# Optimization experiments

Measured on AMD Instinct MI355X. Metric: run time of the kernel, lower is better.

Reference implementation:

```python
import jax, jax.numpy as jnp
import numpy as np

N = 100000      # nodes
E = 1600000     # edges (avg degree 16)
F_IN = 128      # in_feats
H = 128         # n_hidden
C = 40          # n_classes


def setup_inputs() -> dict:
    key = jax.random.key(0)
    ks = jax.random.split(key, 11)
    s = 0.05
    return {
        "x": jax.random.normal(ks[0], (N, F_IN), jnp.float32),
        "edge_index": jax.random.randint(ks[1], (2, E), 0, N, jnp.int32),
        # layer 1: SAGEConv(F_IN, H); lin_l has bias, lin_r has none (PyG default)
        "Wl1": jax.random.normal(ks[2], (F_IN, H), jnp.float32) * s,
        "bl1": jnp.zeros((H,), jnp.float32),
        "Wr1": jax.random.normal(ks[3], (F_IN, H), jnp.float32) * s,
        # layer 2: SAGEConv(H, H)
        "Wl2": jax.random.normal(ks[4], (H, H), jnp.float32) * s,
        "bl2": jnp.zeros((H,), jnp.float32),
        "Wr2": jax.random.normal(ks[5], (H, H), jnp.float32) * s,
        # layer 3: SAGEConv(H, C)
        "Wl3": jax.random.normal(ks[6], (H, C), jnp.float32) * s,
        "bl3": jnp.zeros((C,), jnp.float32),
        "Wr3": jax.random.normal(ks[7], (H, C), jnp.float32) * s,
    }


def _sage_conv(x, src, dst, Wl, bl, Wr):
    # PyG SAGEConv (aggr='mean', root_weight=True):
    #   out[i] = lin_l( mean_{j->i} x[j] ) + lin_r( x[i] )
    msgs = x[src]                                            # [E, d] irregular gather
    agg = jax.ops.segment_sum(msgs, dst, num_segments=N)     # [N, d]
    deg = jax.ops.segment_sum(jnp.ones((src.shape[0], 1), x.dtype), dst,
                              num_segments=N)                # [N, 1]
    agg = agg / jnp.maximum(deg, 1.0)                        # mean aggregation
    return agg @ Wl + bl + x @ Wr


def reference(x, edge_index, Wl1, bl1, Wr1, Wl2, bl2, Wr2, Wl3, bl3, Wr3):
    src, dst = edge_index[0], edge_index[1]
    h = jax.nn.relu(_sage_conv(x, src, dst, Wl1, bl1, Wr1))   # dropout is identity in eval
    h = jax.nn.relu(_sage_conv(h, src, dst, Wl2, bl2, Wr2))
    return _sage_conv(h, src, dst, Wl3, bl3, Wr3)             # [N, C]
```

## Files before the change

### kernel.cpp

```cpp
#include <hip/hip_runtime.h>

using u16 = unsigned short;
using u32 = unsigned int;
using u8 = unsigned char;
typedef __attribute__((ext_vector_type(8))) short short8;
typedef __attribute__((ext_vector_type(4))) float f32x4;

static inline int idiv_up(long a, long b) { return (int)((a + b - 1) / b); }

#define NBUCK 256
#define ECHUNK 8192
#define CAPE 9216

__device__ __forceinline__ float bflo(u32 p) { return __uint_as_float(p << 16); }
__device__ __forceinline__ float bfhi(u32 p) { return __uint_as_float(p & 0xffff0000u); }
__device__ __forceinline__ u32 f2bf1(float f) {
    u32 x = __float_as_uint(f);
    return (x + 0x7fffu + ((x >> 16) & 1u)) >> 16;
}
__device__ __forceinline__ u32 pack2(float lo, float hi) {
    return f2bf1(lo) | (f2bf1(hi) << 16);
}

__global__ __launch_bounds__(256) void k_cast(const float* __restrict__ x,
                                              u32* __restrict__ xb, long nelem) {
    long i = ((long)blockIdx.x * 256 + threadIdx.x) * 8;
    if (i >= nelem) return;
    float4 v0 = *(const float4*)(x + i);
    float4 v1 = *(const float4*)(x + i + 4);
    uint4 o;
    o.x = pack2(v0.x, v0.y);
    o.y = pack2(v0.z, v0.w);
    o.z = pack2(v1.x, v1.y);
    o.w = pack2(v1.z, v1.w);
    *(uint4*)(xb + (i >> 1)) = o;
}

__global__ __launch_bounds__(256) void k_wprepall(const float* __restrict__ Wl1,
                                                  const float* __restrict__ Wr1,
                                                  const float* __restrict__ Wl2,
                                                  const float* __restrict__ Wr2,
                                                  const float* __restrict__ Wl3,
                                                  const float* __restrict__ Wr3,
                                                  u16* __restrict__ wp1,
                                                  u16* __restrict__ wp2,
                                                  u16* __restrict__ wp3) {
    const int b = blockIdx.x;
    if (b < 32) {
        const float* Wl = (b < 16) ? Wl1 : Wl2;
        const float* Wr = (b < 16) ? Wr1 : Wr2;
        u16* wp = (b < 16) ? wp1 : wp2;
        const int gid = (b & 15) * 256 + threadIdx.x;
        const int tile = gid >> 6, l = gid & 63;
        const int t = tile >> 3, s = tile & 7;
        const int n = t * 16 + (l & 15);
        const int k0 = s * 32 + (l >> 4) * 8;
        u32 w[4];
#pragma unroll
        for (int p = 0; p < 4; ++p) {
            const int ka = k0 + 2 * p, kb = ka + 1;
            const float va = (ka < 128) ? Wl[ka * 128 + n] : Wr[(ka - 128) * 128 + n];
            const float vb = (kb < 128) ? Wl[kb * 128 + n] : Wr[(kb - 128) * 128 + n];
            w[p] = pack2(va, vb);
        }
        uint4 o = {w[0], w[1], w[2], w[3]};
        *(uint4*)(wp + (size_t)gid * 8) = o;
    } else {
        const int gid = (b - 32) * 256 + threadIdx.x;
        if (gid >= 20 * 64) return;
        const int tile = gid >> 6, l = gid & 63;
        const int t = tile >> 2, s = tile & 3;
        const int c = t * 16 + (l & 15);
        const int k0 = s * 32 + (l >> 4) * 8;
        u32 w[4];
#pragma unroll
        for (int p = 0; p < 4; ++p) {
            const int ka = k0 + 2 * p, kb = ka + 1;
            const float va = (c < 40) ? Wl3[ka * 40 + c] : Wr3[ka * 40 + (c - 40)];
            const float vb = (c < 40) ? Wl3[kb * 40 + c] : Wr3[kb * 40 + (c - 40)];
            w[p] = pack2(va, vb);
        }
        uint4 o = {w[0], w[1], w[2], w[3]};
        *(uint4*)(wp3 + (size_t)gid * 8) = o;
    }
}

__global__ __launch_bounds__(256) void k_bucket(const int* __restrict__ src,
                                                const int* __restrict__ dst,
                                                int* __restrict__ cursor,
                                                u32* __restrict__ stage,
                                                int E, int rangeSize) {
    __shared__ u32 s_pay[ECHUNK];
    __shared__ u8 s_bk[ECHUNK];
    __shared__ int s_cnt[NBUCK];
    __shared__ int s_base[NBUCK];
    __shared__ int s_off[NBUCK];
    s_cnt[threadIdx.x] = 0;
    __syncthreads();
    const long e0 = (long)blockIdx.x * ECHUNK;
    const int cnt = (int)(((long)E - e0 < ECHUNK) ? (long)E - e0 : ECHUNK);
    for (int j = threadIdx.x; j < cnt; j += 256) {
        const int d = __builtin_nontemporal_load(&dst[e0 + j]);
        const int s = __builtin_nontemporal_load(&src[e0 + j]);
        const int b = d / rangeSize;
        s_pay[j] = (u32)s | ((u32)(d - b * rangeSize) << 17);
        s_bk[j] = (u8)b;
        atomicAdd(&s_cnt[b], 1);
    }
    __syncthreads();
    {
        const int c = s_cnt[threadIdx.x];
        s_base[threadIdx.x] = c ? atomicAdd(&cursor[threadIdx.x], c) : 0;
        s_off[threadIdx.x] = 0;
    }
    __syncthreads();
    for (int j = threadIdx.x; j < cnt; j += 256) {
        const int b = s_bk[j];
        const int p = atomicAdd(&s_off[b], 1);
        stage[(size_t)b * CAPE + s_base[b] + p] = s_pay[j];
    }
}

__global__ __launch_bounds__(256) void k_csrlds(const u32* __restrict__ stage,
                                                const int* __restrict__ cursor,
                                                int* __restrict__ rowptr,
                                                float* __restrict__ invd,
                                                int* __restrict__ col,
                                                int rangeSize, int n) {
    __shared__ int s_cnt[512];
    __shared__ int s_cur[512];
    __shared__ int s_col[CAPE];
    __shared__ int wt[4];
    __shared__ int sh_gbase;
    const int b = blockIdx.x;
    const int t = threadIdx.x;
    const int g0 = b * rangeSize;
    const size_t rd = (size_t)b * CAPE;

    {
        const int v = cursor[t];
        const int lane = t & 63, wid = t >> 6;
        int incl = v;
        for (int off = 1; off < 64; off <<= 1) {
            int u = __shfl_up(incl, off, 64);
            if (lane >= off) incl += u;
        }
        if (lane == 63) wt[wid] = incl;
        __syncthreads();
        int woff = 0;
        for (int w = 0; w < wid; ++w) woff += wt[w];
        if (t == b) sh_gbase = woff + incl - v;
    }
    __syncthreads();
    const int cntb = cursor[b];
    const int gbase = sh_gbase;

    for (int i = t; i < rangeSize; i += 256) s_cnt[i] = 0;
    __syncthreads();

    for (int i = t; i < cntb; i += 256)
        atomicAdd(&s_cnt[stage[rd + i] >> 17], 1);
    __syncthreads();

    const int i0 = 2 * t, i1 = 2 * t + 1;
    const int c0 = (i0 < rangeSize) ? s_cnt[i0] : 0;
    const int c1 = (i1 < rangeSize) ? s_cnt[i1] : 0;
    const int sum = c0 + c1;
    const int lane = t & 63, wid = t >> 6;
    int incl = sum;
    for (int off = 1; off < 64; off <<= 1) {
        int u = __shfl_up(incl, off, 64);
        if (lane >= off) incl += u;
    }
    __syncthreads();
    if (lane == 63) wt[wid] = incl;
    __syncthreads();
    int woff = 0;
    for (int w = 0; w < wid; ++w) woff += wt[w];
    const int excl = woff + incl - sum;
    if (i0 < rangeSize) {
        s_cur[i0] = excl;
        const int g = g0 + i0;
        if (g <= n) rowptr[g] = gbase + excl;
        if (g < n) invd[g] = 1.0f / fmaxf((float)c0, 1.0f);
    }
    if (i1 < rangeSize) {
        s_cur[i1] = excl + c0;
        const int g = g0 + i1;
        if (g <= n) rowptr[g] = gbase + excl + c0;
        if (g < n) invd[g] = 1.0f / fmaxf((float)c1, 1.0f);
    }
    __syncthreads();

    for (int i = t; i < cntb; i += 256) {
        const u32 v = stage[rd + i];
        const int p = atomicAdd(&s_cur[v >> 17], 1);
        s_col[p] = (int)(v & 0x1FFFFu);
    }
    __syncthreads();

    for (int i = t; i < cntb; i += 256) col[gbase + i] = s_col[i];
}

#define ACC4(A, V)                                                     \
    A.x += bflo(V.x); A.y += bfhi(V.x); A.z += bflo(V.y); A.w += bfhi(V.y);

__global__ __launch_bounds__(256, 6) void k_aggmm(const u16* __restrict__ xb,
                                                  const int* __restrict__ rowptr,
                                                  const int* __restrict__ col,
                                                  const float* __restrict__ invd,
                                                  const u16* __restrict__ wp,
                                                  const float* __restrict__ bl,
                                                  u16* __restrict__ outb, int n) {
    __shared__ __align__(16) u16 s_a[64][136];
    const int row0 = blockIdx.x * 64;
    const int tid = threadIdx.x;

    const int l32 = tid & 31;
#pragma unroll
    for (int it = 0; it < 8; ++it) {
        const int r = it * 8 + (tid >> 5);
        const int node = row0 + r;
        float4 a0 = {0.f, 0.f, 0.f, 0.f};
        float4 a1 = {0.f, 0.f, 0.f, 0.f};
        float inv = 0.f;
        if (node < n) {
            inv = invd[node];
            const int s0 = rowptr[node], s1 = rowptr[node + 1];
            for (int cb = s0; cb < s1; cb += 32) {
                const int cnt = min(32, s1 - cb);
                const int cc = (cb + l32 < s1) ? col[cb + l32] : 0;
                int j = 0;
                for (; j + 8 <= cnt; j += 8) {
                    const int n0 = __shfl(cc, j, 32);
                    const int n1 = __shfl(cc, j + 1, 32);
                    const int n2 = __shfl(cc, j + 2, 32);
                    const int n3 = __shfl(cc, j + 3, 32);
                    const int n4 = __shfl(cc, j + 4, 32);
                    const int n5 = __shfl(cc, j + 5, 32);
                    const int n6 = __shfl(cc, j + 6, 32);
                    const int n7 = __shfl(cc, j + 7, 32);
                    const uint2 v0 = *(const uint2*)(xb + (size_t)n0 * 128 + 4 * l32);
                    const uint2 v1 = *(const uint2*)(xb + (size_t)n1 * 128 + 4 * l32);
                    const uint2 v2 = *(const uint2*)(xb + (size_t)n2 * 128 + 4 * l32);
                    const uint2 v3 = *(const uint2*)(xb + (size_t)n3 * 128 + 4 * l32);
                    const uint2 v4 = *(const uint2*)(xb + (size_t)n4 * 128 + 4 * l32);
                    const uint2 v5 = *(const uint2*)(xb + (size_t)n5 * 128 + 4 * l32);
                    const uint2 v6 = *(const uint2*)(xb + (size_t)n6 * 128 + 4 * l32);
                    const uint2 v7 = *(const uint2*)(xb + (size_t)n7 * 128 + 4 * l32);
                    ACC4(a0, v0); ACC4(a1, v1); ACC4(a0, v2); ACC4(a1, v3);
                    ACC4(a0, v4); ACC4(a1, v5); ACC4(a0, v6); ACC4(a1, v7);
                }
                for (; j + 4 <= cnt; j += 4) {
                    const int n0 = __shfl(cc, j, 32);
                    const int n1 = __shfl(cc, j + 1, 32);
                    const int n2 = __shfl(cc, j + 2, 32);
                    const int n3 = __shfl(cc, j + 3, 32);
                    const uint2 v0 = *(const uint2*)(xb + (size_t)n0 * 128 + 4 * l32);
                    const uint2 v1 = *(const uint2*)(xb + (size_t)n1 * 128 + 4 * l32);
                    const uint2 v2 = *(const uint2*)(xb + (size_t)n2 * 128 + 4 * l32);
                    const uint2 v3 = *(const uint2*)(xb + (size_t)n3 * 128 + 4 * l32);
                    ACC4(a0, v0); ACC4(a1, v1); ACC4(a0, v2); ACC4(a1, v3);
                }
                for (; j < cnt; ++j) {
                    const int nn = __shfl(cc, j, 32);
                    const uint2 v = *(const uint2*)(xb + (size_t)nn * 128 + 4 * l32);
                    ACC4(a0, v);
                }
            }
        }
        uint2 o;
        o.x = pack2((a0.x + a1.x) * inv, (a0.y + a1.y) * inv);
        o.y = pack2((a0.z + a1.z) * inv, (a0.w + a1.w) * inv);
        *(uint2*)(&s_a[r][4 * l32]) = o;
    }
    __syncthreads();

    const int l64 = tid & 63;
    const int w = tid >> 6;
    const int rloc = w * 16 + (l64 & 15);
    const int q = l64 >> 4;
    const int rowc = min(row0 + rloc, n - 1);

    f32x4 acc[8];
#pragma unroll
    for (int t = 0; t < 8; ++t) acc[t] = (f32x4){0.f, 0.f, 0.f, 0.f};

#pragma unroll
    for (int s = 0; s < 8; ++s) {
        const short8 a = (s < 4)
            ? *(const short8*)(&s_a[rloc][s * 32 + q * 8])
            : *(const short8*)(xb + (size_t)rowc * 128 + (s - 4) * 32 + q * 8);
#pragma unroll
        for (int t = 0; t < 8; ++t) {
            const short8 b = *(const short8*)(wp + ((size_t)(t * 8 + s) * 64 + l64) * 8);
            acc[t] = __builtin_amdgcn_mfma_f32_16x16x32_bf16(a, b, acc[t], 0, 0, 0);
        }
    }

    const int cb16 = l64 & 15;
    const int rowl = w * 16 + q * 4;
#pragma unroll
    for (int t = 0; t < 8; ++t) {
        const float bias = bl[t * 16 + cb16];
#pragma unroll
        for (int r = 0; r < 4; ++r) {
            const float o = fmaxf(acc[t][r] + bias, 0.f);
            s_a[rowl + r][t * 16 + cb16] = (u16)f2bf1(o);
        }
    }
    __syncthreads();
#pragma unroll
    for (int it = 0; it < 4; ++it) {
        const int idx = tid + it * 256;
        const int r = idx >> 4, c8 = idx & 15;
        const int row = row0 + r;
        if (row < n)
            *(uint4*)(outb + (size_t)row * 128 + c8 * 8) = *(const uint4*)(&s_a[r][c8 * 8]);
    }
}

__global__ __launch_bounds__(256, 4) void k_mm40f(const u16* __restrict__ hb,
                                                  const u16* __restrict__ wp,
                                                  const float* __restrict__ bl,
                                                  u16* __restrict__ t40b,
                                                  float* __restrict__ r40, int n) {
    __shared__ __align__(16) u16 s_a[64][136];
    const int row0 = blockIdx.x * 64;
    const int tid = threadIdx.x;

#pragma unroll
    for (int it = 0; it < 4; ++it) {
        const int idx = tid + it * 256;
        const int r = idx >> 4, c8 = idx & 15;
        const int row = row0 + r;
        uint4 v = {0u, 0u, 0u, 0u};
        if (row < n) v = *(const uint4*)(hb + (size_t)row * 128 + c8 * 8);
        *(uint4*)(&s_a[r][c8 * 8]) = v;
    }
    __syncthreads();

    const int l = tid & 63;
    const int w = tid >> 6;
    const int rloc = w * 16 + (l & 15);
    const int q = l >> 4;

    short8 afr[4];
#pragma unroll
    for (int s = 0; s < 4; ++s)
        afr[s] = *(const short8*)(&s_a[rloc][s * 32 + q * 8]);

    f32x4 acc[5];
#pragma unroll
    for (int t = 0; t < 5; ++t) acc[t] = (f32x4){0.f, 0.f, 0.f, 0.f};

#pragma unroll
    for (int t = 0; t < 5; ++t) {
#pragma unroll
        for (int s = 0; s < 4; ++s) {
            const short8 b = *(const short8*)(wp + ((size_t)(t * 4 + s) * 64 + l) * 8);
            acc[t] = __builtin_amdgcn_mfma_f32_16x16x32_bf16(afr[s], b, acc[t], 0, 0, 0);
        }
    }

    const int rowb = row0 + w * 16 + q * 4;
#pragma unroll
    for (int t = 0; t < 5; ++t) {
        const int c = t * 16 + (l & 15);
        const float bias = (c >= 40) ? bl[c - 40] : 0.f;
#pragma unroll
        for (int r = 0; r < 4; ++r) {
            const int row = rowb + r;
            if (row < n) {
                if (c < 40)
                    t40b[(size_t)row * 40 + c] = (u16)f2bf1(acc[t][r]);
                else
                    r40[(size_t)row * 40 + (c - 40)] = acc[t][r] + bias;
            }
        }
    }
}

__global__ __launch_bounds__(256) void k_agg40(const u16* __restrict__ t40b,
                                               const float* __restrict__ r40,
                                               const int* __restrict__ rowptr,
                                               const int* __restrict__ col,
                                               const float* __restrict__ invd,
                                               float* __restrict__ out, int n) {
    const int tt = blockIdx.x * 256 + threadIdx.x;
    const int node = tt >> 4;
    if (node >= n) return;
    const int l = tt & 15;
    const bool act = l < 10;
    const int s0 = rowptr[node], s1 = rowptr[node + 1];
    float4 a0 = {0.f, 0.f, 0.f, 0.f};
    float4 a1 = {0.f, 0.f, 0.f, 0.f};
    for (int cb = s0; cb < s1; cb += 16) {
        const int cnt = min(16, s1 - cb);
        const int cc = (cb + l < s1) ? col[cb + l] : 0;
        int j = 0;
        for (; j + 4 <= cnt; j += 4) {
            const int n0 = __shfl(cc, j, 16);
            const int n1 = __shfl(cc, j + 1, 16);
            const int n2 = __shfl(cc, j + 2, 16);
            const int n3 = __shfl(cc, j + 3, 16);
            if (act) {
                const uint2 v0 = *(const uint2*)(t40b + (size_t)n0 * 40 + 4 * l);
                const uint2 v1 = *(const uint2*)(t40b + (size_t)n1 * 40 + 4 * l);
                const uint2 v2 = *(const uint2*)(t40b + (size_t)n2 * 40 + 4 * l);
                const uint2 v3 = *(const uint2*)(t40b + (size_t)n3 * 40 + 4 * l);
                ACC4(a0, v0); ACC4(a1, v1); ACC4(a0, v2); ACC4(a1, v3);
            }
        }
        for (; j < cnt; ++j) {
            const int nn = __shfl(cc, j, 16);
            if (act) {
                const uint2 v = *(const uint2*)(t40b + (size_t)nn * 40 + 4 * l);
                ACC4(a0, v);
            }
        }
    }
    if (act) {
        const float inv = invd[node];
        const float4 rv = *(const float4*)(r40 + (size_t)node * 40 + 4 * l);
        float4 o;
        o.x = fmaf(a0.x + a1.x, inv, rv.x);
        o.y = fmaf(a0.y + a1.y, inv, rv.y);
        o.z = fmaf(a0.z + a1.z, inv, rv.z);
        o.w = fmaf(a0.w + a1.w, inv, rv.w);
        *(float4*)(out + (size_t)node * 40 + 4 * l) = o;
    }
}

extern "C" void kernel_launch(void* const* d_in, const int* in_sizes, int n_in,
                              void* d_out, int out_size, void* d_ws, size_t ws_size,
                              hipStream_t stream) {
    const float* x   = (const float*)d_in[0];
    const int*   ei  = (const int*)d_in[1];
    const float* Wl1 = (const float*)d_in[2];
    const float* bl1 = (const float*)d_in[3];
    const float* Wr1 = (const float*)d_in[4];
    const float* Wl2 = (const float*)d_in[5];
    const float* bl2 = (const float*)d_in[6];
    const float* Wr2 = (const float*)d_in[7];
    const float* Wl3 = (const float*)d_in[8];
    const float* bl3 = (const float*)d_in[9];
    const float* Wr3 = (const float*)d_in[10];
    float* out = (float*)d_out;

    const int N = in_sizes[0] / 128;
    const int E = in_sizes[1] / 2;
    const int* src = ei;
    const int* dst = ei + E;

    auto align1k = [](size_t v) { return (v + 1023) & ~(size_t)1023; };
    const size_t NB16 = (size_t)N * 128 * sizeof(u16);

    char* ws = (char*)d_ws;
    size_t off = 0;
    float* invd     = (float*)(ws + off); off += align1k((size_t)N * 4);
    int*   rowptr   = (int*)(ws + off);   off += align1k((size_t)(N + 1) * 4);
    int*   cursor   = (int*)(ws + off);   off += align1k(NBUCK * 4);
    u16*   wp1      = (u16*)(ws + off);   off += align1k(64 * 1024);
    u16*   wp2      = (u16*)(ws + off);   off += align1k(64 * 1024);
    u16*   wp3      = (u16*)(ws + off);   off += align1k(20 * 1024);
    int*   col      = (int*)(ws + off);   off += align1k((size_t)E * 4);
    u32*   stage    = (u32*)(ws + off);   off += align1k((size_t)NBUCK * CAPE * 4);
    u16*   xb       = (u16*)(ws + off);   off += align1k(NB16);
    char*  regionY  = (ws + off);         off += align1k(NB16);
    u16*   h1b  = (u16*)regionY;
    u16*   h2b  = xb;
    u16*   t40b = (u16*)regionY;
    float* r40  = (float*)(regionY + align1k((size_t)N * 40 * sizeof(u16)));

    const int nPB        = idiv_up(E, ECHUNK);
    const int castBlocks = idiv_up((long)N * 128, 2048);
    const int agg40Blk   = idiv_up((long)N * 16, 256);
    const int mmBlocks   = idiv_up(N, 64);
    const int rangeSize  = idiv_up(N, NBUCK);

    k_cast<<<castBlocks, 256, 0, stream>>>(x, (u32*)xb, (long)N * 128);
    k_wprepall<<<37, 256, 0, stream>>>(Wl1, Wr1, Wl2, Wr2, Wl3, Wr3, wp1, wp2, wp3);

    hipMemsetAsync(cursor, 0, NBUCK * sizeof(int), stream);
    k_bucket<<<nPB, 256, 0, stream>>>(src, dst, cursor, stage, E, rangeSize);
    k_csrlds<<<NBUCK, 256, 0, stream>>>(stage, cursor, rowptr, invd, col,
                                        rangeSize, N);

    k_aggmm<<<mmBlocks, 256, 0, stream>>>(xb, rowptr, col, invd, wp1, bl1, h1b, N);

    k_aggmm<<<mmBlocks, 256, 0, stream>>>(h1b, rowptr, col, invd, wp2, bl2, h2b, N);

    k_mm40f<<<mmBlocks, 256, 0, stream>>>(h2b, wp3, bl3, t40b, r40, N);
    k_agg40<<<agg40Blk, 256, 0, stream>>>(t40b, r40, rowptr, col, invd, out, N);
}
```

Measured before the change: 294.8 us.

## Split fused aggregate+matmul into separate gather and MFMA GEMM kernels

Replaces the fused k_aggmm kernel with a standalone neighbor-mean aggregation kernel (one half-wave per node, no LDS) that writes a bf16 intermediate, followed by a separate MFMA GEMM kernel that stages agg and root features in LDS. This decouples the latency-bound gather from the MFMA work so the gather can run at full occupancy without LDS limits. In exchange it adds an extra N×128 bf16 write and read per layer and two more kernel launches, and the GEMM now writes outputs with scattered 2-byte stores.

```diff
diff --git a/kernel.cpp b/kernel.cpp
--- a/kernel.cpp
+++ b/kernel.cpp
@@ -205,118 +205,124 @@
 #define ACC4(A, V)                                                     \
     A.x += bflo(V.x); A.y += bfhi(V.x); A.z += bflo(V.y); A.w += bfhi(V.y);
 
-__global__ __launch_bounds__(256, 6) void k_aggmm(const u16* __restrict__ xb,
-                                                  const int* __restrict__ rowptr,
-                                                  const int* __restrict__ col,
-                                                  const float* __restrict__ invd,
-                                                  const u16* __restrict__ wp,
-                                                  const float* __restrict__ bl,
-                                                  u16* __restrict__ outb, int n) {
-    __shared__ __align__(16) u16 s_a[64][136];
+__global__ __launch_bounds__(256) void k_aggb(const u16* __restrict__ xb,
+                                              const int* __restrict__ rowptr,
+                                              const int* __restrict__ col,
+                                              const float* __restrict__ invd,
+                                              u16* __restrict__ aggb, int n) {
+    const int t = blockIdx.x * 256 + threadIdx.x;
+    const int node = t >> 5;
+    if (node >= n) return;
+    const int l = t & 31;
+    const int s0 = rowptr[node], s1 = rowptr[node + 1];
+    float4 a0 = {0.f, 0.f, 0.f, 0.f};
+    float4 a1 = {0.f, 0.f, 0.f, 0.f};
+    for (int cb = s0; cb < s1; cb += 32) {
+        const int cnt = min(32, s1 - cb);
+        const int cc = (cb + l < s1) ? col[cb + l] : 0;
+        int j = 0;
+        for (; j + 8 <= cnt; j += 8) {
+            const int n0 = __shfl(cc, j, 32);
+            const int n1 = __shfl(cc, j + 1, 32);
+            const int n2 = __shfl(cc, j + 2, 32);
+            const int n3 = __shfl(cc, j + 3, 32);
+            const int n4 = __shfl(cc, j + 4, 32);
+            const int n5 = __shfl(cc, j + 5, 32);
+            const int n6 = __shfl(cc, j + 6, 32);
+            const int n7 = __shfl(cc, j + 7, 32);
+            const uint2 v0 = *(const uint2*)(xb + (size_t)n0 * 128 + 4 * l);
+            const uint2 v1 = *(const uint2*)(xb + (size_t)n1 * 128 + 4 * l);
+            const uint2 v2 = *(const uint2*)(xb + (size_t)n2 * 128 + 4 * l);
+            const uint2 v3 = *(const uint2*)(xb + (size_t)n3 * 128 + 4 * l);
+            const uint2 v4 = *(const uint2*)(xb + (size_t)n4 * 128 + 4 * l);
+            const uint2 v5 = *(const uint2*)(xb + (size_t)n5 * 128 + 4 * l);
+            const uint2 v6 = *(const uint2*)(xb + (size_t)n6 * 128 + 4 * l);
+            const uint2 v7 = *(const uint2*)(xb + (size_t)n7 * 128 + 4 * l);
+            ACC4(a0, v0); ACC4(a1, v1); ACC4(a0, v2); ACC4(a1, v3);
+            ACC4(a0, v4); ACC4(a1, v5); ACC4(a0, v6); ACC4(a1, v7);
+        }
+        for (; j + 4 <= cnt; j += 4) {
+            const int n0 = __shfl(cc, j, 32);
+            const int n1 = __shfl(cc, j + 1, 32);
+            const int n2 = __shfl(cc, j + 2, 32);
+            const int n3 = __shfl(cc, j + 3, 32);
+            const uint2 v0 = *(const uint2*)(xb + (size_t)n0 * 128 + 4 * l);
+            const uint2 v1 = *(const uint2*)(xb + (size_t)n1 * 128 + 4 * l);
+            const uint2 v2 = *(const uint2*)(xb + (size_t)n2 * 128 + 4 * l);
+            const uint2 v3 = *(const uint2*)(xb + (size_t)n3 * 128 + 4 * l);
+            ACC4(a0, v0); ACC4(a1, v1); ACC4(a0, v2); ACC4(a1, v3);
+        }
+        for (; j < cnt; ++j) {
+            const int nn = __shfl(cc, j, 32);
+            const uint2 v = *(const uint2*)(xb + (size_t)nn * 128 + 4 * l);
+            ACC4(a0, v);
+        }
+    }
+    const float inv = invd[node];
+    uint2 o;
+    o.x = pack2((a0.x + a1.x) * inv, (a0.y + a1.y) * inv);
+    o.y = pack2((a0.z + a1.z) * inv, (a0.w + a1.w) * inv);
+    *(uint2*)(aggb + (size_t)node * 128 + 4 * l) = o;
+}
+
+__global__ __launch_bounds__(256, 4) void k_mmf(const u16* __restrict__ aggb,
+                                                const u16* __restrict__ xrb,
+                                                const u16* __restrict__ wp,
+                                                const float* __restrict__ bl,
+                                                u16* __restrict__ outb, int n) {
+    __shared__ __align__(16) u16 s_a[64][264];
     const int row0 = blockIdx.x * 64;
     const int tid = threadIdx.x;
 
-    const int l32 = tid & 31;
 #pragma unroll
     for (int it = 0; it < 8; ++it) {
-        const int r = it * 8 + (tid >> 5);
-        const int node = row0 + r;
-        float4 a0 = {0.f, 0.f, 0.f, 0.f};
-        float4 a1 = {0.f, 0.f, 0.f, 0.f};
-        float inv = 0.f;
-        if (node < n) {
-            inv = invd[node];
-            const int s0 = rowptr[node], s1 = rowptr[node + 1];
-            for (int cb = s0; cb < s1; cb += 32) {
-                const int cnt = min(32, s1 - cb);
-                const int cc = (cb + l32 < s1) ? col[cb + l32] : 0;
-                int j = 0;
-                for (; j + 8 <= cnt; j += 8) {
-                    const int n0 = __shfl(cc, j, 32);
-                    const int n1 = __shfl(cc, j + 1, 32);
-                    const int n2 = __shfl(cc, j + 2, 32);
-                    const int n3 = __shfl(cc, j + 3, 32);
-                    const int n4 = __shfl(cc, j + 4, 32);
-                    const int n5 = __shfl(cc, j + 5, 32);
-                    const int n6 = __shfl(cc, j + 6, 32);
-                    const int n7 = __shfl(cc, j + 7, 32);
-                    const uint2 v0 = *(const uint2*)(xb + (size_t)n0 * 128 + 4 * l32);
-                    const uint2 v1 = *(const uint2*)(xb + (size_t)n1 * 128 + 4 * l32);
-                    const uint2 v2 = *(const uint2*)(xb + (size_t)n2 * 128 + 4 * l32);
-                    const uint2 v3 = *(const uint2*)(xb + (size_t)n3 * 128 + 4 * l32);
-                    const uint2 v4 = *(const uint2*)(xb + (size_t)n4 * 128 + 4 * l32);
-                    const uint2 v5 = *(const uint2*)(xb + (size_t)n5 * 128 + 4 * l32);
-                    const uint2 v6 = *(const uint2*)(xb + (size_t)n6 * 128 + 4 * l32);
-                    const uint2 v7 = *(const uint2*)(xb + (size_t)n7 * 128 + 4 * l32);
-                    ACC4(a0, v0); ACC4(a1, v1); ACC4(a0, v2); ACC4(a1, v3);
-                    ACC4(a0, v4); ACC4(a1, v5); ACC4(a0, v6); ACC4(a1, v7);
-                }
-                for (; j + 4 <= cnt; j += 4) {
-                    const int n0 = __shfl(cc, j, 32);
-                    const int n1 = __shfl(cc, j + 1, 32);
-                    const int n2 = __shfl(cc, j + 2, 32);
-                    const int n3 = __shfl(cc, j + 3, 32);
-                    const uint2 v0 = *(const uint2*)(xb + (size_t)n0 * 128 + 4 * l32);
-                    const uint2 v1 = *(const uint2*)(xb + (size_t)n1 * 128 + 4 * l32);
-                    const uint2 v2 = *(const uint2*)(xb + (size_t)n2 * 128 + 4 * l32);
-                    const uint2 v3 = *(const uint2*)(xb + (size_t)n3 * 128 + 4 * l32);
-                    ACC4(a0, v0); ACC4(a1, v1); ACC4(a0, v2); ACC4(a1, v3);
-                }
-                for (; j < cnt; ++j) {
-                    const int nn = __shfl(cc, j, 32);
-                    const uint2 v = *(const uint2*)(xb + (size_t)nn * 128 + 4 * l32);
-                    ACC4(a0, v);
-                }
+        const int idx = tid + it * 256;
+        const int r = idx >> 5, c8 = idx & 31;
+        const int row = row0 + r;
+        uint4 v = {0u, 0u, 0u, 0u};
+        if (row < n) {
+            v = (c8 < 16) ? *(const uint4*)(aggb + (size_t)row * 128 + c8 * 8)
+                          : *(const uint4*)(xrb + (size_t)row * 128 + (c8 - 16) * 8);
+        }
+        *(uint4*)(&s_a[r][c8 * 8]) = v;
+    }
+    __syncthreads();
+
+    const int l = tid & 63;
+    const int w = tid >> 6;
+    const int rloc = w * 16 + (l & 15);
+    const int q = l >> 4;
+
+    short8 afr[8];
+#pragma unroll
+    for (int s = 0; s < 8; ++s)
+        afr[s] = *(const short8*)(&s_a[rloc][s * 32 + q * 8]);
+
+    f32x4 acc[8];
+#pragma unroll
+    for (int t = 0; t < 8; ++t) acc[t] = (f32x4){0.f, 0.f, 0.f, 0.f};
+
+#pragma unroll
+    for (int t = 0; t < 8; ++t) {
+#pragma unroll
+        for (int s = 0; s < 8; ++s) {
+            const short8 b = *(const short8*)(wp + ((size_t)(t * 8 + s) * 64 + l) * 8);
+            acc[t] = __builtin_amdgcn_mfma_f32_16x16x32_bf16(afr[s], b, acc[t], 0, 0, 0);
+        }
+    }
+
+    const int rowb = row0 + w * 16 + q * 4;
+#pragma unroll
+    for (int t = 0; t < 8; ++t) {
+        const float bias = bl[t * 16 + (l & 15)];
+#pragma unroll
+        for (int r = 0; r < 4; ++r) {
+            const int row = rowb + r;
+            if (row < n) {
+                const float o = fmaxf(acc[t][r] + bias, 0.f);
+                outb[(size_t)row * 128 + t * 16 + (l & 15)] = (u16)f2bf1(o);
             }
         }
-        uint2 o;
-        o.x = pack2((a0.x + a1.x) * inv, (a0.y + a1.y) * inv);
-        o.y = pack2((a0.z + a1.z) * inv, (a0.w + a1.w) * inv);
-        *(uint2*)(&s_a[r][4 * l32]) = o;
-    }
-    __syncthreads();
-
-    const int l64 = tid & 63;
-    const int w = tid >> 6;
-    const int rloc = w * 16 + (l64 & 15);
-    const int q = l64 >> 4;
-    const int rowc = min(row0 + rloc, n - 1);
-
-    f32x4 acc[8];
-#pragma unroll
-    for (int t = 0; t < 8; ++t) acc[t] = (f32x4){0.f, 0.f, 0.f, 0.f};
-
-#pragma unroll
-    for (int s = 0; s < 8; ++s) {
-        const short8 a = (s < 4)
-            ? *(const short8*)(&s_a[rloc][s * 32 + q * 8])
-            : *(const short8*)(xb + (size_t)rowc * 128 + (s - 4) * 32 + q * 8);
-#pragma unroll
-        for (int t = 0; t < 8; ++t) {
-            const short8 b = *(const short8*)(wp + ((size_t)(t * 8 + s) * 64 + l64) * 8);
-            acc[t] = __builtin_amdgcn_mfma_f32_16x16x32_bf16(a, b, acc[t], 0, 0, 0);
-        }
-    }
-
-    const int cb16 = l64 & 15;
-    const int rowl = w * 16 + q * 4;
-#pragma unroll
-    for (int t = 0; t < 8; ++t) {
-        const float bias = bl[t * 16 + cb16];
-#pragma unroll
-        for (int r = 0; r < 4; ++r) {
-            const float o = fmaxf(acc[t][r] + bias, 0.f);
-            s_a[rowl + r][t * 16 + cb16] = (u16)f2bf1(o);
-        }
-    }
-    __syncthreads();
-#pragma unroll
-    for (int it = 0; it < 4; ++it) {
-        const int idx = tid + it * 256;
-        const int r = idx >> 4, c8 = idx & 15;
-        const int row = row0 + r;
-        if (row < n)
-            *(uint4*)(outb + (size_t)row * 128 + c8 * 8) = *(const uint4*)(&s_a[r][c8 * 8]);
     }
 }
 
@@ -466,6 +472,7 @@
     u16*   wp3      = (u16*)(ws + off);   off += align1k(20 * 1024);
     int*   col      = (int*)(ws + off);   off += align1k((size_t)E * 4);
     u32*   stage    = (u32*)(ws + off);   off += align1k((size_t)NBUCK * CAPE * 4);
+    u16*   aggb     = (u16*)(ws + off);   off += align1k(NB16);
     u16*   xb       = (u16*)(ws + off);   off += align1k(NB16);
     char*  regionY  = (ws + off);         off += align1k(NB16);
     u16*   h1b  = (u16*)regionY;
@@ -475,6 +482,7 @@
 
     const int nPB        = idiv_up(E, ECHUNK);
     const int castBlocks = idiv_up((long)N * 128, 2048);
+    const int aggBlocks  = idiv_up((long)N * 32, 256);
     const int agg40Blk   = idiv_up((long)N * 16, 256);
     const int mmBlocks   = idiv_up(N, 64);
     const int rangeSize  = idiv_up(N, NBUCK);
@@ -487,9 +495,11 @@
     k_csrlds<<<NBUCK, 256, 0, stream>>>(stage, cursor, rowptr, invd, col,
                                         rangeSize, N);
 
-    k_aggmm<<<mmBlocks, 256, 0, stream>>>(xb, rowptr, col, invd, wp1, bl1, h1b, N);
-
-    k_aggmm<<<mmBlocks, 256, 0, stream>>>(h1b, rowptr, col, invd, wp2, bl2, h2b, N);
+    k_aggb<<<aggBlocks, 256, 0, stream>>>(xb, rowptr, col, invd, aggb, N);
+    k_mmf<<<mmBlocks, 256, 0, stream>>>(aggb, xb, wp1, bl1, h1b, N);
+
+    k_aggb<<<aggBlocks, 256, 0, stream>>>(h1b, rowptr, col, invd, aggb, N);
+    k_mmf<<<mmBlocks, 256, 0, stream>>>(aggb, h1b, wp2, bl2, h2b, N);
 
     k_mm40f<<<mmBlocks, 256, 0, stream>>>(h2b, wp3, bl3, t40b, r40, N);
     k_agg40<<<agg40Blk, 256, 0, stream>>>(t40b, r40, rowptr, col, invd, out, N);
```

Result: no change. 291.3 us (-1.2%).
